# Kernel tuning notes

Hardware: AMD Instinct MI355X
Metric: run time of the kernel (lower is better)

Reference implementation:

```python
import jax, jax.numpy as jnp
import numpy as np

ALPHAS = (0.1, 0.3, 0.5)
WEIGHTS = (0.5, 0.3, 0.2)

B, T, D = 32, 8192, 64


def setup_inputs() -> dict:
    key = jax.random.key(0)
    k1, k2 = jax.random.split(key)
    pred = jax.random.normal(k1, (B, T, D), dtype=jnp.float32)
    target = jax.random.normal(k2, (B, T, D), dtype=jnp.float32)
    return {"pred": pred, "target": target}


def _ema(x, alpha):
    # ema_0 = x_0 ; ema_i = alpha*x_i + (1-alpha)*ema_{i-1}
    # Express each step as affine op (mult, add) and compose with an
    # associative scan along the time axis (dim=1):  y_i = mult*y_{i-1} + add.
    mult = jnp.full(x.shape, 1.0 - alpha, dtype=x.dtype).at[:, 0].set(0.0)
    add = (alpha * x).at[:, 0].set(x[:, 0])

    def combine(c1, c2):  # apply c1 first, then c2
        a1, b1 = c1
        a2, b2 = c2
        return (a1 * a2, b1 * a2 + b2)

    _, ema = jax.lax.associative_scan(combine, (mult, add), axis=1)
    return ema


def _scale_loss(pred, target, alpha):
    pe = _ema(pred, alpha)   # [B, T, D]
    te = _ema(target, alpha)
    pd = pe[:, 1:] - pe[:, :-1]
    td = te[:, 1:] - te[:, :-1]
    mismatch = jnp.sign(pd) != jnp.sign(td)
    step_err = jnp.square(pe[:, 1:] - te[:, 1:])
    masked = jnp.where(mismatch, step_err, jnp.zeros_like(step_err))
    return masked.mean(axis=1)  # [B, D]


def reference(pred, target):
    loss = sum(w * _scale_loss(pred, target, a) for a, w in zip(ALPHAS, WEIGHTS))
    return loss.mean()  # reduction='mean'
```

## Files before the change

kernel.cpp:

```cpp
#include <hip/hip_runtime.h>


namespace {
constexpr int BB  = 32;
constexpr int TT  = 8192;
constexpr int DD  = 64;
constexpr int CH  = 32;
constexpr int WU  = 32;
constexpr int NCH = TT / CH;
constexpr int WPB = 4;
constexpr int BT  = 16;
constexpr float INV_NORM = 1.0f / (8191.0f * 2048.0f);
}

__global__ void zero_out_kernel(float* o) { o[0] = 0.0f; }

__device__ __forceinline__ void load16(const float* __restrict__ p,
                                       const float* __restrict__ q, int bt,
                                       float (&xs)[BT], float (&ys)[BT]) {
#pragma unroll
  for (int i = 0; i < BT; ++i) {
    xs[i] = p[(bt + i) * DD];
    ys[i] = q[(bt + i) * DD];
  }
}

__device__ __forceinline__ void warm16_a0(const float (&xs)[BT], const float (&ys)[BT],
                                          float& pe0, float& te0) {
#pragma unroll
  for (int i = 0; i < BT; ++i) {
    pe0 = fmaf(0.1f, xs[i] - pe0, pe0);
    te0 = fmaf(0.1f, ys[i] - te0, te0);
  }
}

__device__ __forceinline__ void warm16_all(const float (&xs)[BT], const float (&ys)[BT],
    float& pe0, float& te0, float& pe1, float& te1, float& pe2, float& te2) {
#pragma unroll
  for (int i = 0; i < BT; ++i) {
    pe0 = fmaf(0.1f, xs[i] - pe0, pe0);  te0 = fmaf(0.1f, ys[i] - te0, te0);
    pe1 = fmaf(0.3f, xs[i] - pe1, pe1);  te1 = fmaf(0.3f, ys[i] - te1, te1);
    pe2 = fmaf(0.5f, xs[i] - pe2, pe2);  te2 = fmaf(0.5f, ys[i] - te2, te2);
  }
}

__device__ __forceinline__ void step1(float xx, float yy, float a, float w,
                                      float& pe, float& te, float& acc) {
  float dx = xx - pe;
  float dy = yy - te;
  pe = fmaf(a, dx, pe);
  te = fmaf(a, dy, te);
  float e   = pe - te;
  float sel = (dx * dy < 0.0f) ? w : 0.0f;
  acc = fmaf(sel, e * e, acc);
}

__device__ __forceinline__ void acc16_all(const float (&xs)[BT], const float (&ys)[BT],
    float& pe0, float& te0, float& pe1, float& te1, float& pe2, float& te2,
    float& acc) {
#pragma unroll
  for (int i = 0; i < BT; ++i) {
    step1(xs[i], ys[i], 0.1f, 0.5f, pe0, te0, acc);
    step1(xs[i], ys[i], 0.3f, 0.3f, pe1, te1, acc);
    step1(xs[i], ys[i], 0.5f, 0.2f, pe2, te2, acc);
  }
}

__global__ __launch_bounds__(256, 8) void ms_trend_loss_kernel(
    const float* __restrict__ pred, const float* __restrict__ targ,
    float* __restrict__ out) {
  const int lane = threadIdx.x & 63;
  const int wave = threadIdx.x >> 6;
  const int unit = blockIdx.x * WPB + wave;
  const int b = unit >> 8;
  const int c = unit & 255;
  const int s = c * CH;
  const int start = (c == 0) ? 0 : (s - WU);

  const float* p = pred + (b * TT + start) * DD + lane;
  const float* q = targ + (b * TT + start) * DD + lane;

  float pe0, pe1, pe2, te0, te1, te2;
  float acc = 0.0f;
  float xs[BT], ys[BT];

  if (c == 0) {
    load16(p, q, 0, xs, ys);
    pe0 = pe1 = pe2 = xs[0];
    te0 = te1 = te2 = ys[0];
    acc16_all(xs, ys, pe0, te0, pe1, te1, pe2, te2, acc);
    load16(p, q, BT, xs, ys);
    acc16_all(xs, ys, pe0, te0, pe1, te1, pe2, te2, acc);
  } else {
    load16(p, q, 0, xs, ys);
    pe0 = xs[0];
    te0 = ys[0];
    warm16_a0(xs, ys, pe0, te0);
    load16(p, q, BT, xs, ys);
    pe1 = pe2 = xs[0];
    te1 = te2 = ys[0];
    warm16_all(xs, ys, pe0, te0, pe1, te1, pe2, te2);
    load16(p, q, 2 * BT, xs, ys);
    acc16_all(xs, ys, pe0, te0, pe1, te1, pe2, te2, acc);
    load16(p, q, 3 * BT, xs, ys);
    acc16_all(xs, ys, pe0, te0, pe1, te1, pe2, te2, acc);
  }

#pragma unroll
  for (int off = 32; off > 0; off >>= 1) acc += __shfl_down(acc, off);
  __shared__ float sred[WPB];
  if (lane == 0) sred[wave] = acc;
  __syncthreads();
  if (threadIdx.x == 0) {
    float t = sred[0] + sred[1] + sred[2] + sred[3];
    atomicAdd(out, t * INV_NORM);
  }
}

extern "C" void kernel_launch(void* const* d_in, const int* in_sizes, int n_in,
                              void* d_out, int out_size, void* d_ws, size_t ws_size,
                              hipStream_t stream) {
  (void)in_sizes; (void)n_in; (void)out_size; (void)d_ws; (void)ws_size;
  const float* pred = (const float*)d_in[0];
  const float* targ = (const float*)d_in[1];
  float* out = (float*)d_out;

  zero_out_kernel<<<1, 1, 0, stream>>>(out);
  ms_trend_loss_kernel<<<BB * NCH / WPB, 256, 0, stream>>>(pred, targ, out);
}
```

Baseline: 158.7 us.

## Double chunk length and double-buffer register loads in EMA trend loss

Each wave now covers 64 time steps instead of 32, while the warm-up window stays at 32 steps. That cuts the share of redundant warm-up loads and EMA work per useful output. The loads are also split across two register buffers, so the next 16-step slab is fetched while the current one is computed. The cost is more registers per thread (launch bounds relaxed from 8 to 4), half as many waves for latency hiding, and a longer serial chain per wave.

```diff
diff --git a/kernel.cpp b/kernel.cpp
--- a/kernel.cpp
+++ b/kernel.cpp
@@ -5,7 +5,7 @@
 constexpr int BB  = 32;
 constexpr int TT  = 8192;
 constexpr int DD  = 64;
-constexpr int CH  = 32;
+constexpr int CH  = 64;
 constexpr int WU  = 32;
 constexpr int NCH = TT / CH;
 constexpr int WPB = 4;
@@ -66,14 +66,14 @@
   }
 }
 
-__global__ __launch_bounds__(256, 8) void ms_trend_loss_kernel(
+__global__ __launch_bounds__(256, 4) void ms_trend_loss_kernel(
     const float* __restrict__ pred, const float* __restrict__ targ,
     float* __restrict__ out) {
   const int lane = threadIdx.x & 63;
   const int wave = threadIdx.x >> 6;
   const int unit = blockIdx.x * WPB + wave;
-  const int b = unit >> 8;
-  const int c = unit & 255;
+  const int b = unit >> 7;
+  const int c = unit & 127;
   const int s = c * CH;
   const int start = (c == 0) ? 0 : (s - WU);
 
@@ -82,28 +82,36 @@
 
   float pe0, pe1, pe2, te0, te1, te2;
   float acc = 0.0f;
-  float xs[BT], ys[BT];
+  float xa[BT], ya[BT], xb[BT], yb[BT];
 
   if (c == 0) {
-    load16(p, q, 0, xs, ys);
-    pe0 = pe1 = pe2 = xs[0];
-    te0 = te1 = te2 = ys[0];
-    acc16_all(xs, ys, pe0, te0, pe1, te1, pe2, te2, acc);
-    load16(p, q, BT, xs, ys);
-    acc16_all(xs, ys, pe0, te0, pe1, te1, pe2, te2, acc);
+    load16(p, q, 0, xa, ya);
+    load16(p, q, BT, xb, yb);
+    pe0 = pe1 = pe2 = xa[0];
+    te0 = te1 = te2 = ya[0];
+    acc16_all(xa, ya, pe0, te0, pe1, te1, pe2, te2, acc);
+    load16(p, q, 2 * BT, xa, ya);
+    acc16_all(xb, yb, pe0, te0, pe1, te1, pe2, te2, acc);
+    load16(p, q, 3 * BT, xb, yb);
+    acc16_all(xa, ya, pe0, te0, pe1, te1, pe2, te2, acc);
+    acc16_all(xb, yb, pe0, te0, pe1, te1, pe2, te2, acc);
   } else {
-    load16(p, q, 0, xs, ys);
-    pe0 = xs[0];
-    te0 = ys[0];
-    warm16_a0(xs, ys, pe0, te0);
-    load16(p, q, BT, xs, ys);
-    pe1 = pe2 = xs[0];
-    te1 = te2 = ys[0];
-    warm16_all(xs, ys, pe0, te0, pe1, te1, pe2, te2);
-    load16(p, q, 2 * BT, xs, ys);
-    acc16_all(xs, ys, pe0, te0, pe1, te1, pe2, te2, acc);
-    load16(p, q, 3 * BT, xs, ys);
-    acc16_all(xs, ys, pe0, te0, pe1, te1, pe2, te2, acc);
+    load16(p, q, 0, xa, ya);
+    load16(p, q, BT, xb, yb);
+    pe0 = xa[0];
+    te0 = ya[0];
+    warm16_a0(xa, ya, pe0, te0);
+    load16(p, q, 2 * BT, xa, ya);
+    pe1 = pe2 = xb[0];
+    te1 = te2 = yb[0];
+    warm16_all(xb, yb, pe0, te0, pe1, te1, pe2, te2);
+    load16(p, q, 3 * BT, xb, yb);
+    acc16_all(xa, ya, pe0, te0, pe1, te1, pe2, te2, acc);
+    load16(p, q, 4 * BT, xa, ya);
+    acc16_all(xb, yb, pe0, te0, pe1, te1, pe2, te2, acc);
+    load16(p, q, 5 * BT, xb, yb);
+    acc16_all(xa, ya, pe0, te0, pe1, te1, pe2, te2, acc);
+    acc16_all(xb, yb, pe0, te0, pe1, te1, pe2, te2, acc);
   }
 
 #pragma unroll
```

Result: faster. 148.1 us (-6.7%).
